# Performance work log

Measured on AMD Instinct MI355X. Metric: run time of the kernel, lower is better.

The kernel has to match this reference:

```python
import jax, jax.numpy as jnp
import numpy as np

HEADS = 16
DIM_HEAD = 64
SEG = 512            # total_segment_len (num_longterm_mem_tokens = 0)
THETA = 10000.0
NEG_INF = -1e30


def _rotate_half(t):
    # interleaved pair rotation, as in rotary-embedding-torch
    t2 = t.reshape(*t.shape[:-1], t.shape[-1] // 2, 2)
    return jnp.stack((-t2[..., 1], t2[..., 0]), axis=-1).reshape(t.shape)


def setup_inputs() -> dict:
    key = jax.random.key(0)
    ks = jax.random.split(key, 4)
    b, n, d = 2, 4096, 1024
    dim_inner = HEADS * DIM_HEAD
    seq = jax.random.normal(ks[0], (b, n, d), dtype=jnp.float32)
    g_norm = jnp.ones((d,), dtype=jnp.float32)
    W_qkv = jax.random.normal(ks[1], (d, 3 * dim_inner), dtype=jnp.float32) * (d ** -0.5)
    W_out = jax.random.normal(ks[2], (dim_inner, d), dtype=jnp.float32) * (dim_inner ** -0.5)
    pm = jax.random.normal(ks[3], (2, HEADS, 16, DIM_HEAD), dtype=jnp.float32) * 0.02
    return {"seq": seq, "g_norm": g_norm, "W_qkv": W_qkv, "W_out": W_out, "pm": pm}


def reference(seq, g_norm, W_qkv, W_out, pm):
    b, n_tot, dim = seq.shape
    p = pm.shape[2]
    dh = DIM_HEAD

    # RMSNorm (elementwise affine, eps = dtype eps as in torch default)
    eps = jnp.asarray(jnp.finfo(seq.dtype).eps, seq.dtype)
    x = seq * jax.lax.rsqrt(jnp.mean(seq * seq, axis=-1, keepdims=True) + eps) * g_norm

    qkv = x @ W_qkv                                   # [b, n, 3*h*dh]
    q, k, v = jnp.split(qkv, 3, axis=-1)

    def split_heads(t):
        return t.reshape(b, n_tot, HEADS, dh).transpose(0, 2, 1, 3)  # b h n d

    q, k, v = map(split_heads, (q, k, v))

    # rotary over global positions (applied before segmenting)
    pos = jnp.arange(n_tot, dtype=seq.dtype)
    inv_freq = 1.0 / (THETA ** (jnp.arange(0, dh, 2, dtype=seq.dtype) / dh))
    ang = jnp.repeat(pos[:, None] * inv_freq, 2, axis=-1)            # [n, dh]
    cos, sin = jnp.cos(ang), jnp.sin(ang)
    q = q * cos + _rotate_half(q) * sin
    k = k * cos + _rotate_half(k) * sin

    # fold segments into batch: b h (w n) d -> (b w) h n d
    w = n_tot // SEG
    def seg_fold(t):
        return t.reshape(b, HEADS, w, SEG, dh).transpose(0, 2, 1, 3, 4).reshape(b * w, HEADS, SEG, dh)
    q, k, v = map(seg_fold, (q, k, v))

    # prepend persistent memory kv
    pmk = jnp.broadcast_to(pm[0], (b * w, HEADS, p, dh))
    pmv = jnp.broadcast_to(pm[1], (b * w, HEADS, p, dh))
    k = jnp.concatenate((pmk, k), axis=-2)            # [(bw), h, p+n, d]
    v = jnp.concatenate((pmv, v), axis=-2)

    scores = jnp.einsum('bhid,bhjd->bhij', q, k) * (dh ** -0.5)
    i = jnp.arange(SEG)[:, None]
    j = jnp.arange(SEG + p)[None, :]
    mask = (j < p) | ((j - p) <= i)                   # persistent mem always visible, causal in-segment
    scores = jnp.where(mask, scores, NEG_INF)
    attn = jax.nn.softmax(scores, axis=-1)
    out = jnp.einsum('bhij,bhjd->bhid', attn, v)      # [(bw), h, n, d]

    out = out.transpose(0, 2, 1, 3).reshape(b * w, SEG, HEADS * dh)
    out = out @ W_out
    return out.reshape(b, n_tot, dim)
```

## Files before the change

### kernel.cpp

```cpp
#include <hip/hip_runtime.h>
#include <hip/hip_bf16.h>

typedef __attribute__((ext_vector_type(8))) short short8v;
typedef __attribute__((ext_vector_type(4))) float f32x4;

#define B_ 2
#define NTOK 4096
#define DMODEL 1024
#define HEADS_ 16
#define DH 64
#define SEG_ 512
#define PMEM 16
#define ROWS 8192
#define QKVC 3072

__global__ __launch_bounds__(256) void rmsnorm_bf16(const float* __restrict__ seq,
                                                    const float* __restrict__ g,
                                                    __hip_bfloat16* __restrict__ x) {
    int row = blockIdx.x;
    const float4* in = (const float4*)(seq + (size_t)row * DMODEL);
    int tid = threadIdx.x;
    float4 v = in[tid];
    float ss = v.x*v.x + v.y*v.y + v.z*v.z + v.w*v.w;
    #pragma unroll
    for (int off = 32; off >= 1; off >>= 1) ss += __shfl_xor(ss, off, 64);
    __shared__ float red[4];
    if ((tid & 63) == 0) red[tid >> 6] = ss;
    __syncthreads();
    float tot = red[0] + red[1] + red[2] + red[3];
    float scale = rsqrtf(tot * (1.0f/(float)DMODEL) + 1.1920929e-7f);
    float4 gv = ((const float4*)g)[tid];
    union { ushort4 u; __hip_bfloat16 h[4]; } pk;
    pk.h[0] = __float2bfloat16(v.x*scale*gv.x);
    pk.h[1] = __float2bfloat16(v.y*scale*gv.y);
    pk.h[2] = __float2bfloat16(v.z*scale*gv.z);
    pk.h[3] = __float2bfloat16(v.w*scale*gv.w);
    ((ushort4*)(x + (size_t)row * DMODEL))[tid] = pk.u;
}

__global__ __launch_bounds__(256) void setup_kernel(float* __restrict__ tab,
                                                    const float* __restrict__ pm,
                                                    __hip_bfloat16* __restrict__ pmb,
                                                    const float* __restrict__ wqkv,
                                                    __hip_bfloat16* __restrict__ wqkvt,
                                                    const float* __restrict__ wout,
                                                    __hip_bfloat16* __restrict__ woutt) {
    __shared__ float t[32][33];
    int b = blockIdx.x;
    if (b < 640) {
        int idx = b*256 + threadIdx.x;
        if (idx < NTOK*32) {
            int n = idx >> 5, p = idx & 31;
            float inv = powf(10000.f, -(float)p * (1.f/32.f));
            float a = (float)n * inv;
            float sn, cs;
            sincosf(a, &sn, &cs);
            tab[(size_t)n*64 + 2*p]     = cs;
            tab[(size_t)n*64 + 2*p + 1] = sn;
        } else {
            int j = idx - NTOK*32;
            pmb[j] = __float2bfloat16(pm[j]);
        }
        return;
    }
    b -= 640;
    const float* W; __hip_bfloat16* Wt; int N, n0, k0;
    if (b < 3072) { W = wqkv; Wt = wqkvt; N = QKVC;   n0 = (b % 96)*32; k0 = (b / 96)*32; }
    else { b -= 3072; W = wout; Wt = woutt; N = DMODEL; n0 = (b % 32)*32; k0 = (b / 32)*32; }
    int c = threadIdx.x & 31, r = threadIdx.x >> 5;
    #pragma unroll
    for (int rr = 0; rr < 32; rr += 8)
        t[rr + r][c] = W[(size_t)(k0 + rr + r)*N + n0 + c];
    __syncthreads();
    #pragma unroll
    for (int rr = 0; rr < 32; rr += 8)
        Wt[(size_t)(n0 + rr + r)*DMODEL + k0 + c] = __float2bfloat16(t[c][rr + r]);
}

__device__ __forceinline__ void gldl(const __hip_bfloat16* g, char* l) {
    __builtin_amdgcn_global_load_lds((const __attribute__((address_space(1))) void*)g,
                                     (__attribute__((address_space(3))) void*)l, 16, 0, 0);
}
__device__ __forceinline__ void storeC(float* p, float v) { *p = v; }
__device__ __forceinline__ void storeC(__hip_bfloat16* p, float v) { *p = __float2bfloat16(v); }

template<typename OutT, bool ROPE>
__global__ __launch_bounds__(256, 2) void gemm_t(const __hip_bfloat16* __restrict__ A,
                                                 const __hip_bfloat16* __restrict__ Bt,
                                                 OutT* __restrict__ C,
                                                 const float* __restrict__ tab,
                                                 int M, int N, int K) {
    __shared__ __align__(16) char smem[32768];
    const int tid = threadIdx.x;
    const int wid = tid >> 6, lane = tid & 63;
    const int q8 = gridDim.x >> 3;
    const int swz = (blockIdx.x & 7) * q8 + (blockIdx.x >> 3);
    const int nbx = N >> 7;
    const int bm = (swz / nbx) * 128, bn = (swz % nbx) * 128;
    const int wm = (wid >> 1) * 64, wn = (wid & 1) * 64;
    const int fr = lane & 15, g = lane >> 4;

    const int srow = tid >> 3;
    const int scol = ((tid & 7) ^ (srow & 7)) * 8;
    const __hip_bfloat16* Asrc = A  + (size_t)(bm + srow)*K + scol;
    const __hip_bfloat16* Bsrc = Bt + (size_t)(bn + srow)*K + scol;

    f32x4 acc[4][4];
    #pragma unroll
    for (int i = 0; i < 4; ++i)
        #pragma unroll
        for (int j = 0; j < 4; ++j)
            acc[i][j] = (f32x4){0.f, 0.f, 0.f, 0.f};

    for (int k0 = 0; k0 < K; k0 += 64) {
        #pragma unroll
        for (int i = 0; i < 4; ++i)
            gldl(Asrc + (size_t)i*32*K + k0, smem + i*4096 + tid*16);
        #pragma unroll
        for (int i = 0; i < 4; ++i)
            gldl(Bsrc + (size_t)i*32*K + k0, smem + 16384 + i*4096 + tid*16);
        __syncthreads();

        short8v a[4][2], b[4][2];
        #pragma unroll
        for (int mt = 0; mt < 4; ++mt) {
            int row = wm + mt*16 + fr;
            #pragma unroll
            for (int ks = 0; ks < 2; ++ks)
                a[mt][ks] = *(const short8v*)(smem + row*128 + ((ks*64 + g*16) ^ ((fr&7)<<4)));
        }
        #pragma unroll
        for (int nt = 0; nt < 4; ++nt) {
            int row = wn + nt*16 + fr;
            #pragma unroll
            for (int ks = 0; ks < 2; ++ks)
                b[nt][ks] = *(const short8v*)(smem + 16384 + row*128 + ((ks*64 + g*16) ^ ((fr&7)<<4)));
        }
        #pragma unroll
        for (int mt = 0; mt < 4; ++mt)
            #pragma unroll
            for (int nt = 0; nt < 4; ++nt)
                #pragma unroll
                for (int ks = 0; ks < 2; ++ks)
                    acc[mt][nt] = __builtin_amdgcn_mfma_f32_16x16x32_bf16(a[mt][ks], b[nt][ks], acc[mt][nt], 0, 0, 0);
        __syncthreads();
    }

    const int rsub = (lane >> 4) << 2;
    if (ROPE && bn < 2048) {
        #pragma unroll
        for (int mt = 0; mt < 4; ++mt) {
            int rbase = bm + wm + mt*16 + rsub;
            #pragma unroll
            for (int nt = 0; nt < 4; ++nt) {
                int col = bn + wn + nt*16 + fr;
                int d = col & 63;
                int dc = d & ~1;
                #pragma unroll
                for (int r = 0; r < 4; ++r) {
                    float v = acc[mt][nt][r];
                    float pv = __shfl_xor(v, 1, 64);
                    int n = (rbase + r) & (NTOK - 1);
                    const float* tb = tab + (size_t)n*64;
                    float cs = tb[dc], sn = tb[dc+1];
                    float o = v*cs + ((d & 1) ? pv*sn : -pv*sn);
                    storeC(&C[(size_t)(rbase + r)*N + col], (float)o);
                }
            }
        }
    } else {
        #pragma unroll
        for (int mt = 0; mt < 4; ++mt) {
            int rbase = bm + wm + mt*16 + rsub;
            #pragma unroll
            for (int nt = 0; nt < 4; ++nt) {
                int col = bn + wn + nt*16 + fr;
                #pragma unroll
                for (int r = 0; r < 4; ++r)
                    storeC(&C[(size_t)(rbase + r)*N + col], acc[mt][nt][r]);
            }
        }
    }
}

__device__ __forceinline__ void stage_load(const __hip_bfloat16* __restrict__ qkv,
                                           const __hip_bfloat16* __restrict__ pmb,
                                           int h, int srow, int tt, int skey, int sdg,
                                           uint4 kv[2]) {
    int kg = tt*64 + skey;
    if (kg < PMEM) {
        kv[0] = *(const uint4*)(pmb + ((size_t)h*PMEM + kg)*DH + sdg);
        kv[1] = *(const uint4*)(pmb + ((size_t)(HEADS_ + h)*PMEM + kg)*DH + sdg);
    } else {
        int r = min(kg - PMEM, SEG_ - 1);
        const __hip_bfloat16* bp = qkv + (size_t)(srow + r)*QKVC + h*DH + sdg;
        kv[0] = *(const uint4*)(bp + 1024);
        kv[1] = *(const uint4*)(bp + 2048);
    }
}

__device__ __forceinline__ void stage_write(char* Kb, char* Vb,
                                            int skey, int sdg, const uint4 kv[2]) {
    *(uint4*)(Kb + ((skey*128 + sdg*2) ^ ((skey&7)<<4))) = kv[0];
    union { uint4 u; ushort s[8]; } vv; vv.u = kv[1];
    #pragma unroll
    for (int j = 0; j < 8; ++j) {
        int d = sdg + j;
        *(ushort*)(Vb + ((d*128 + skey*2) ^ ((d&7)<<4))) = vv.s[j];
    }
}

__global__ __launch_bounds__(512, 2) void attn_mfma(const __hip_bfloat16* __restrict__ qkv,
                                                    const __hip_bfloat16* __restrict__ pmb,
                                                    __hip_bfloat16* __restrict__ ao) {
    __shared__ __hip_bfloat16 KB[2][4096];
    __shared__ __hip_bfloat16 VB[2][4096];
    __shared__ __hip_bfloat16 PB[8][1024];

    const int bid = blockIdx.x;
    const int xcd = bid & 7, ii = bid >> 3;
    const int s  = 2*xcd + (ii >> 5);
    const int h  = ii & 15;
    const int rb = (ii >> 4) & 1;
    const int srow = (s >> 3)*NTOK + (s & 7)*SEG_;
    const int tid = threadIdx.x;
    const int w = tid >> 6, lane = tid & 63;
    const int g = lane >> 4, fr = lane & 15;
    const int rsub = g * 4;
    char* Pw = (char*)&PB[w][0];

    const int grp0 = 2*w + rb;
    const int grp1 = 30 - 2*w + rb;
    const int tmax = 7 + rb;

    short8v aq[2][2];
    #pragma unroll
    for (int mt = 0; mt < 2; ++mt) {
        int grp = mt ? grp1 : grp0;
        const __hip_bfloat16* qp = qkv + (size_t)(srow + grp*16 + fr)*QKVC + h*DH;
        #pragma unroll
        for (int ks = 0; ks < 2; ++ks)
            aq[mt][ks] = *(const short8v*)(qp + ks*32 + g*8);
    }

    f32x4 accO[2][4];
    float l_[2][4];
    #pragma unroll
    for (int mt = 0; mt < 2; ++mt) {
        #pragma unroll
        for (int dt = 0; dt < 4; ++dt) accO[mt][dt] = (f32x4){0.f,0.f,0.f,0.f};
        #pragma unroll
        for (int r = 0; r < 4; ++r) l_[mt][r] = 0.f;
    }

    const int skey = tid >> 3, sdg = (tid & 7) * 8;

    {
        uint4 kv[2];
        stage_load(qkv, pmb, h, srow, 0, skey, sdg, kv);
        stage_write((char*)&KB[0][0], (char*)&VB[0][0], skey, sdg, kv);
    }
    __syncthreads();

    for (int t = 0; t <= tmax; ++t) {
        const int bf = t & 1;
        uint4 kvn[2];
        if (t < tmax) stage_load(qkv, pmb, h, srow, t + 1, skey, sdg, kvn);

        char* Kb = (char*)&KB[bf][0];
        char* Vb = (char*)&VB[bf][0];

        short8v bk[4][2];
        #pragma unroll
        for (int nt = 0; nt < 4; ++nt)
            #pragma unroll
            for (int ks = 0; ks < 2; ++ks) {
                int row = nt*16 + fr;
                bk[nt][ks] = *(const short8v*)(Kb + ((row*128 + ks*64 + g*16) ^ ((row&7)<<4)));
            }

        #pragma unroll
        for (int mt = 0; mt < 2; ++mt) {
            const int qb = (mt ? grp1 : grp0) * 16;
            if (t > 0 && t*64 > qb + 31) continue;

            f32x4 sA[4];
            #pragma unroll
            for (int nt = 0; nt < 4; ++nt) sA[nt] = (f32x4){0.f,0.f,0.f,0.f};
            __builtin_amdgcn_s_setprio(1);
            #pragma unroll
            for (int ks = 0; ks < 2; ++ks)
                #pragma unroll
                for (int nt = 0; nt < 4; ++nt)
                    sA[nt] = __builtin_amdgcn_mfma_f32_16x16x32_bf16(aq[mt][ks], bk[nt][ks], sA[nt], 0, 0, 0);
            __builtin_amdgcn_s_setprio(0);

            if (!(t*64 + 63 <= qb + 16)) {
                #pragma unroll
                for (int nt = 0; nt < 4; ++nt) {
                    int kg2 = t*64 + nt*16 + fr;
                    #pragma unroll
                    for (int r = 0; r < 4; ++r) {
                        int irow = qb + rsub + r;
                        if (!((kg2 < PMEM) || (kg2 <= irow + PMEM))) sA[nt][r] = -1e30f;
                    }
                }
            }

            #pragma unroll
            for (int nt = 0; nt < 4; ++nt)
                #pragma unroll
                for (int r = 0; r < 4; ++r)
                    sA[nt][r] = __expf(fmaf(sA[nt][r], 0.125f, -8.0f));
            #pragma unroll
            for (int r = 0; r < 4; ++r)
                l_[mt][r] += sA[0][r] + sA[1][r] + sA[2][r] + sA[3][r];

            #pragma unroll
            for (int nt = 0; nt < 4; ++nt)
                #pragma unroll
                for (int r = 0; r < 4; ++r) {
                    int row_l = rsub + r;
                    *(__hip_bfloat16*)(Pw + ((row_l*128 + (nt*16 + fr)*2) ^ ((row_l&7)<<4))) =
                        __float2bfloat16(sA[nt][r]);
                }

            __builtin_amdgcn_s_setprio(1);
            #pragma unroll
            for (int ks2 = 0; ks2 < 2; ++ks2) {
                short8v ap = *(const short8v*)(Pw + ((fr*128 + ks2*64 + g*16) ^ ((fr&7)<<4)));
                #pragma unroll
                for (int dt = 0; dt < 4; ++dt) {
                    int vrow = dt*16 + fr;
                    short8v bv = *(const short8v*)(Vb + ((vrow*128 + ks2*64 + g*16) ^ ((vrow&7)<<4)));
                    accO[mt][dt] = __builtin_amdgcn_mfma_f32_16x16x32_bf16(ap, bv, accO[mt][dt], 0, 0, 0);
                }
            }
            __builtin_amdgcn_s_setprio(0);
        }

        if (t < tmax) stage_write((char*)&KB[bf^1][0], (char*)&VB[bf^1][0], skey, sdg, kvn);
        __syncthreads();
    }

    #pragma unroll
    for (int mt = 0; mt < 2; ++mt) {
        const int grp = mt ? grp1 : grp0;
        float inv[4];
        #pragma unroll
        for (int r = 0; r < 4; ++r) {
            float lt = l_[mt][r];
            #pragma unroll
            for (int off = 1; off <= 8; off <<= 1) lt += __shfl_xor(lt, off, 64);
            inv[r] = 1.0f / lt;
        }
        #pragma unroll
        for (int dt = 0; dt < 4; ++dt)
            #pragma unroll
            for (int r = 0; r < 4; ++r) {
                int row_l = rsub + r;
                *(__hip_bfloat16*)(Pw + ((row_l*128 + (dt*16 + fr)*2) ^ ((row_l&7)<<4))) =
                    __float2bfloat16(accO[mt][dt][r] * inv[r]);
            }
        #pragma unroll
        for (int c = 0; c < 2; ++c) {
            int row_l = c*8 + (lane >> 3);
            size_t grow = (size_t)(srow + grp*16 + row_l);
            uint4 v = *(const uint4*)(Pw + ((row_l*128 + (lane&7)*16) ^ ((row_l&7)<<4)));
            *(uint4*)((char*)(ao + grow*DMODEL + h*DH) + (lane&7)*16) = v;
        }
    }
}

extern "C" void kernel_launch(void* const* d_in, const int* in_sizes, int n_in,
                              void* d_out, int out_size, void* d_ws, size_t ws_size,
                              hipStream_t stream) {
    const float* seq  = (const float*)d_in[0];
    const float* g    = (const float*)d_in[1];
    const float* wqkv = (const float*)d_in[2];
    const float* wout = (const float*)d_in[3];
    const float* pm   = (const float*)d_in[4];
    float* out = (float*)d_out;

    char* ws = (char*)d_ws;
    __hip_bfloat16* qkvb  = (__hip_bfloat16*)ws;
    __hip_bfloat16* xb    = (__hip_bfloat16*)(ws + 50331648);
    __hip_bfloat16* wqkvt = (__hip_bfloat16*)(ws + 50331648 + 16777216);
    __hip_bfloat16* woutt = (__hip_bfloat16*)(ws + 50331648 + 16777216 + 6291456);
    float* tab            = (float*)(ws + 50331648 + 16777216 + 6291456 + 2097152);
    __hip_bfloat16* pmb   = (__hip_bfloat16*)(ws + 50331648 + 16777216 + 6291456 + 2097152 + 1048576);

    setup_kernel<<<4736, 256, 0, stream>>>(tab, pm, pmb, wqkv, wqkvt, wout, woutt);
    rmsnorm_bf16<<<ROWS, 256, 0, stream>>>(seq, g, xb);
    gemm_t<__hip_bfloat16, true><<<(QKVC/128)*(ROWS/128), 256, 0, stream>>>(xb, wqkvt, qkvb, tab, ROWS, QKVC, DMODEL);
    attn_mfma<<<512, 512, 0, stream>>>(qkvb, pmb, xb);
    gemm_t<float, false><<<(DMODEL/128)*(ROWS/128), 256, 0, stream>>>(xb, woutt, out, nullptr, ROWS, DMODEL, DMODEL);
}
```

Before: 147.9 us.

## Merge setup and RMSNorm launches; stage 128-key K/V tiles in attention

Folds the one-time setup kernel and the RMSNorm kernel into a single launch, using block-index ranges to pick the role, which removes one launch and its inter-kernel gap. The attention kernel now stages 128 keys per pipeline step as two 64-key halves, so the number of loop iterations and __syncthreads barriers is halved. Each thread loads twice as much K/V per stage. Shared memory per block doubles to about 80 KB, which may limit occupancy at two blocks per CU.

```diff
diff --git a/kernel.cpp b/kernel.cpp
--- a/kernel.cpp
+++ b/kernel.cpp
@@ -14,49 +14,51 @@
 #define ROWS 8192
 #define QKVC 3072
 
-__global__ __launch_bounds__(256) void rmsnorm_bf16(const float* __restrict__ seq,
-                                                    const float* __restrict__ g,
-                                                    __hip_bfloat16* __restrict__ x) {
-    int row = blockIdx.x;
-    const float4* in = (const float4*)(seq + (size_t)row * DMODEL);
+__global__ __launch_bounds__(256) void prep_all(float* __restrict__ tab,
+                                                const float* __restrict__ pm,
+                                                __hip_bfloat16* __restrict__ pmb,
+                                                const float* __restrict__ wqkv,
+                                                __hip_bfloat16* __restrict__ wqkvt,
+                                                const float* __restrict__ wout,
+                                                __hip_bfloat16* __restrict__ woutt,
+                                                const float* __restrict__ seq,
+                                                const float* __restrict__ g,
+                                                __hip_bfloat16* __restrict__ x) {
+    __shared__ float t[32][33];
+    __shared__ float red[4];
+    int b = blockIdx.x;
     int tid = threadIdx.x;
-    float4 v = in[tid];
-    float ss = v.x*v.x + v.y*v.y + v.z*v.z + v.w*v.w;
-    #pragma unroll
-    for (int off = 32; off >= 1; off >>= 1) ss += __shfl_xor(ss, off, 64);
-    __shared__ float red[4];
-    if ((tid & 63) == 0) red[tid >> 6] = ss;
-    __syncthreads();
-    float tot = red[0] + red[1] + red[2] + red[3];
-    float scale = rsqrtf(tot * (1.0f/(float)DMODEL) + 1.1920929e-7f);
-    float4 gv = ((const float4*)g)[tid];
-    union { ushort4 u; __hip_bfloat16 h[4]; } pk;
-    pk.h[0] = __float2bfloat16(v.x*scale*gv.x);
-    pk.h[1] = __float2bfloat16(v.y*scale*gv.y);
-    pk.h[2] = __float2bfloat16(v.z*scale*gv.z);
-    pk.h[3] = __float2bfloat16(v.w*scale*gv.w);
-    ((ushort4*)(x + (size_t)row * DMODEL))[tid] = pk.u;
-}
-
-__global__ __launch_bounds__(256) void setup_kernel(float* __restrict__ tab,
-                                                    const float* __restrict__ pm,
-                                                    __hip_bfloat16* __restrict__ pmb,
-                                                    const float* __restrict__ wqkv,
-                                                    __hip_bfloat16* __restrict__ wqkvt,
-                                                    const float* __restrict__ wout,
-                                                    __hip_bfloat16* __restrict__ woutt) {
-    __shared__ float t[32][33];
-    int b = blockIdx.x;
+    if (b >= 4736) {
+        int row = b - 4736;
+        const float4* in = (const float4*)(seq + (size_t)row * DMODEL);
+        float4 v = in[tid];
+        float ss = v.x*v.x + v.y*v.y + v.z*v.z + v.w*v.w;
+        #pragma unroll
+        for (int off = 32; off >= 1; off >>= 1) ss += __shfl_xor(ss, off, 64);
+        if ((tid & 63) == 0) red[tid >> 6] = ss;
+        __syncthreads();
+        float tot = red[0] + red[1] + red[2] + red[3];
+        float scale = rsqrtf(tot * (1.0f/(float)DMODEL) + 1.1920929e-7f);
+        float4 gv = ((const float4*)g)[tid];
+        union { ushort4 u; __hip_bfloat16 h[4]; } pk;
+        pk.h[0] = __float2bfloat16(v.x*scale*gv.x);
+        pk.h[1] = __float2bfloat16(v.y*scale*gv.y);
+        pk.h[2] = __float2bfloat16(v.z*scale*gv.z);
+        pk.h[3] = __float2bfloat16(v.w*scale*gv.w);
+        ((ushort4*)(x + (size_t)row * DMODEL))[tid] = pk.u;
+        return;
+    }
     if (b < 640) {
-        int idx = b*256 + threadIdx.x;
+        int idx = b*256 + tid;
         if (idx < NTOK*32) {
             int n = idx >> 5, p = idx & 31;
             float inv = powf(10000.f, -(float)p * (1.f/32.f));
             float a = (float)n * inv;
             float sn, cs;
             sincosf(a, &sn, &cs);
-            tab[(size_t)n*64 + 2*p]     = cs;
-            tab[(size_t)n*64 + 2*p + 1] = sn;
+            float* tp = tab + (size_t)n*64;
+            tp[2*p]     = cs;
+            tp[2*p + 1] = sn;
         } else {
             int j = idx - NTOK*32;
             pmb[j] = __float2bfloat16(pm[j]);
@@ -67,7 +69,7 @@
     const float* W; __hip_bfloat16* Wt; int N, n0, k0;
     if (b < 3072) { W = wqkv; Wt = wqkvt; N = QKVC;   n0 = (b % 96)*32; k0 = (b / 96)*32; }
     else { b -= 3072; W = wout; Wt = woutt; N = DMODEL; n0 = (b % 32)*32; k0 = (b / 32)*32; }
-    int c = threadIdx.x & 31, r = threadIdx.x >> 5;
+    int c = tid & 31, r = tid >> 5;
     #pragma unroll
     for (int rr = 0; rr < 32; rr += 8)
         t[rr + r][c] = W[(size_t)(k0 + rr + r)*N + n0 + c];
@@ -186,35 +188,42 @@
 __device__ __forceinline__ void stage_load(const __hip_bfloat16* __restrict__ qkv,
                                            const __hip_bfloat16* __restrict__ pmb,
                                            int h, int srow, int tt, int skey, int sdg,
-                                           uint4 kv[2]) {
-    int kg = tt*64 + skey;
+                                           uint4 kv[4]) {
+    int kg = tt*128 + skey;
     if (kg < PMEM) {
-        kv[0] = *(const uint4*)(pmb + ((size_t)h*PMEM + kg)*DH + sdg);
-        kv[1] = *(const uint4*)(pmb + ((size_t)(HEADS_ + h)*PMEM + kg)*DH + sdg);
+        const __hip_bfloat16* kp = pmb + ((size_t)h*PMEM + kg)*DH + sdg;
+        const __hip_bfloat16* vp = pmb + ((size_t)(HEADS_ + h)*PMEM + kg)*DH + sdg;
+        kv[0] = *(const uint4*)kp;      kv[1] = *(const uint4*)(kp + 8);
+        kv[2] = *(const uint4*)vp;      kv[3] = *(const uint4*)(vp + 8);
     } else {
         int r = min(kg - PMEM, SEG_ - 1);
         const __hip_bfloat16* bp = qkv + (size_t)(srow + r)*QKVC + h*DH + sdg;
-        kv[0] = *(const uint4*)(bp + 1024);
-        kv[1] = *(const uint4*)(bp + 2048);
+        kv[0] = *(const uint4*)(bp + 1024); kv[1] = *(const uint4*)(bp + 1032);
+        kv[2] = *(const uint4*)(bp + 2048); kv[3] = *(const uint4*)(bp + 2056);
     }
 }
 
 __device__ __forceinline__ void stage_write(char* Kb, char* Vb,
-                                            int skey, int sdg, const uint4 kv[2]) {
-    *(uint4*)(Kb + ((skey*128 + sdg*2) ^ ((skey&7)<<4))) = kv[0];
-    union { uint4 u; ushort s[8]; } vv; vv.u = kv[1];
-    #pragma unroll
-    for (int j = 0; j < 8; ++j) {
+                                            int skey, int sdg, const uint4 kv[4]) {
+    int half = skey >> 6, row = skey & 63;
+    char* Kh = Kb + half*8192;
+    int b0 = row*128 + sdg*2;
+    *(uint4*)(Kh + ((b0)      ^ ((row&7)<<4))) = kv[0];
+    *(uint4*)(Kh + ((b0 + 16) ^ ((row&7)<<4))) = kv[1];
+    char* Vh = Vb + half*8192;
+    union { uint4 u[2]; ushort s[16]; } vv; vv.u[0] = kv[2]; vv.u[1] = kv[3];
+    #pragma unroll
+    for (int j = 0; j < 16; ++j) {
         int d = sdg + j;
-        *(ushort*)(Vb + ((d*128 + skey*2) ^ ((d&7)<<4))) = vv.s[j];
+        *(ushort*)(Vh + ((d*128 + row*2) ^ ((d&7)<<4))) = vv.s[j];
     }
 }
 
 __global__ __launch_bounds__(512, 2) void attn_mfma(const __hip_bfloat16* __restrict__ qkv,
                                                     const __hip_bfloat16* __restrict__ pmb,
                                                     __hip_bfloat16* __restrict__ ao) {
-    __shared__ __hip_bfloat16 KB[2][4096];
-    __shared__ __hip_bfloat16 VB[2][4096];
+    __shared__ __hip_bfloat16 KB[2][8192];
+    __shared__ __hip_bfloat16 VB[2][8192];
     __shared__ __hip_bfloat16 PB[8][1024];
 
     const int bid = blockIdx.x;
@@ -231,7 +240,7 @@
 
     const int grp0 = 2*w + rb;
     const int grp1 = 30 - 2*w + rb;
-    const int tmax = 7 + rb;
+    const int tmax = 3 + rb;
 
     short8v aq[2][2];
     #pragma unroll
@@ -253,10 +262,10 @@
         for (int r = 0; r < 4; ++r) l_[mt][r] = 0.f;
     }
 
-    const int skey = tid >> 3, sdg = (tid & 7) * 8;
+    const int skey = tid >> 2, sdg = (tid & 3) * 16;
 
     {
-        uint4 kv[2];
+        uint4 kv[4];
         stage_load(qkv, pmb, h, srow, 0, skey, sdg, kv);
         stage_write((char*)&KB[0][0], (char*)&VB[0][0], skey, sdg, kv);
     }
@@ -264,79 +273,83 @@
 
     for (int t = 0; t <= tmax; ++t) {
         const int bf = t & 1;
-        uint4 kvn[2];
+        uint4 kvn[4];
         if (t < tmax) stage_load(qkv, pmb, h, srow, t + 1, skey, sdg, kvn);
 
-        char* Kb = (char*)&KB[bf][0];
-        char* Vb = (char*)&VB[bf][0];
-
-        short8v bk[4][2];
-        #pragma unroll
-        for (int nt = 0; nt < 4; ++nt)
-            #pragma unroll
-            for (int ks = 0; ks < 2; ++ks) {
-                int row = nt*16 + fr;
-                bk[nt][ks] = *(const short8v*)(Kb + ((row*128 + ks*64 + g*16) ^ ((row&7)<<4)));
-            }
-
-        #pragma unroll
-        for (int mt = 0; mt < 2; ++mt) {
-            const int qb = (mt ? grp1 : grp0) * 16;
-            if (t > 0 && t*64 > qb + 31) continue;
-
-            f32x4 sA[4];
-            #pragma unroll
-            for (int nt = 0; nt < 4; ++nt) sA[nt] = (f32x4){0.f,0.f,0.f,0.f};
-            __builtin_amdgcn_s_setprio(1);
-            #pragma unroll
-            for (int ks = 0; ks < 2; ++ks)
+        #pragma unroll
+        for (int hs = 0; hs < 2; ++hs) {
+            char* Kb = (char*)&KB[bf][0] + hs*8192;
+            char* Vb = (char*)&VB[bf][0] + hs*8192;
+            const int base = t*128 + hs*64;
+
+            short8v bk[4][2];
+            #pragma unroll
+            for (int nt = 0; nt < 4; ++nt)
+                #pragma unroll
+                for (int ks = 0; ks < 2; ++ks) {
+                    int row = nt*16 + fr;
+                    bk[nt][ks] = *(const short8v*)(Kb + ((row*128 + ks*64 + g*16) ^ ((row&7)<<4)));
+                }
+
+            #pragma unroll
+            for (int mt = 0; mt < 2; ++mt) {
+                const int qb = (mt ? grp1 : grp0) * 16;
+                if (base > 0 && base > qb + 31) continue;
+
+                f32x4 sA[4];
+                #pragma unroll
+                for (int nt = 0; nt < 4; ++nt) sA[nt] = (f32x4){0.f,0.f,0.f,0.f};
+                __builtin_amdgcn_s_setprio(1);
+                #pragma unroll
+                for (int ks = 0; ks < 2; ++ks)
+                    #pragma unroll
+                    for (int nt = 0; nt < 4; ++nt)
+                        sA[nt] = __builtin_amdgcn_mfma_f32_16x16x32_bf16(aq[mt][ks], bk[nt][ks], sA[nt], 0, 0, 0);
+                __builtin_amdgcn_s_setprio(0);
+
+                if (!(base + 63 <= qb + 16)) {
+                    #pragma unroll
+                    for (int nt = 0; nt < 4; ++nt) {
+                        int kg2 = base + nt*16 + fr;
+                        #pragma unroll
+                        for (int r = 0; r < 4; ++r) {
+                            int irow = qb + rsub + r;
+                            if (!((kg2 < PMEM) || (kg2 <= irow + PMEM))) sA[nt][r] = -1e30f;
+                        }
+                    }
+                }
+
                 #pragma unroll
                 for (int nt = 0; nt < 4; ++nt)
-                    sA[nt] = __builtin_amdgcn_mfma_f32_16x16x32_bf16(aq[mt][ks], bk[nt][ks], sA[nt], 0, 0, 0);
-            __builtin_amdgcn_s_setprio(0);
-
-            if (!(t*64 + 63 <= qb + 16)) {
-                #pragma unroll
-                for (int nt = 0; nt < 4; ++nt) {
-                    int kg2 = t*64 + nt*16 + fr;
+                    #pragma unroll
+                    for (int r = 0; r < 4; ++r)
+                        sA[nt][r] = __expf(fmaf(sA[nt][r], 0.125f, -8.0f));
+                #pragma unroll
+                for (int r = 0; r < 4; ++r)
+                    l_[mt][r] += sA[0][r] + sA[1][r] + sA[2][r] + sA[3][r];
+
+                #pragma unroll
+                for (int nt = 0; nt < 4; ++nt)
                     #pragma unroll
                     for (int r = 0; r < 4; ++r) {
-                        int irow = qb + rsub + r;
-                        if (!((kg2 < PMEM) || (kg2 <= irow + PMEM))) sA[nt][r] = -1e30f;
+                        int row_l = rsub + r;
+                        *(__hip_bfloat16*)(Pw + ((row_l*128 + (nt*16 + fr)*2) ^ ((row_l&7)<<4))) =
+                            __float2bfloat16(sA[nt][r]);
+                    }
+
+                __builtin_amdgcn_s_setprio(1);
+                #pragma unroll
+                for (int ks2 = 0; ks2 < 2; ++ks2) {
+                    short8v ap = *(const short8v*)(Pw + ((fr*128 + ks2*64 + g*16) ^ ((fr&7)<<4)));
+                    #pragma unroll
+                    for (int dt = 0; dt < 4; ++dt) {
+                        int vrow = dt*16 + fr;
+                        short8v bv = *(const short8v*)(Vb + ((vrow*128 + ks2*64 + g*16) ^ ((vrow&7)<<4)));
+                        accO[mt][dt] = __builtin_amdgcn_mfma_f32_16x16x32_bf16(ap, bv, accO[mt][dt], 0, 0, 0);
                     }
                 }
+                __builtin_amdgcn_s_setprio(0);
             }
-
-            #pragma unroll
-            for (int nt = 0; nt < 4; ++nt)
-                #pragma unroll
-                for (int r = 0; r < 4; ++r)
-                    sA[nt][r] = __expf(fmaf(sA[nt][r], 0.125f, -8.0f));
-            #pragma unroll
-            for (int r = 0; r < 4; ++r)
-                l_[mt][r] += sA[0][r] + sA[1][r] + sA[2][r] + sA[3][r];
-
-            #pragma unroll
-            for (int nt = 0; nt < 4; ++nt)
-                #pragma unroll
-                for (int r = 0; r < 4; ++r) {
-                    int row_l = rsub + r;
-                    *(__hip_bfloat16*)(Pw + ((row_l*128 + (nt*16 + fr)*2) ^ ((row_l&7)<<4))) =
-                        __float2bfloat16(sA[nt][r]);
-                }
-
-            __builtin_amdgcn_s_setprio(1);
-            #pragma unroll
-            for (int ks2 = 0; ks2 < 2; ++ks2) {
-                short8v ap = *(const short8v*)(Pw + ((fr*128 + ks2*64 + g*16) ^ ((fr&7)<<4)));
-                #pragma unroll
-                for (int dt = 0; dt < 4; ++dt) {
-                    int vrow = dt*16 + fr;
-                    short8v bv = *(const short8v*)(Vb + ((vrow*128 + ks2*64 + g*16) ^ ((vrow&7)<<4)));
-                    accO[mt][dt] = __builtin_amdgcn_mfma_f32_16x16x32_bf16(ap, bv, accO[mt][dt], 0, 0, 0);
-                }
-            }
-            __builtin_amdgcn_s_setprio(0);
         }
 
         if (t < tmax) stage_write((char*)&KB[bf^1][0], (char*)&VB[bf^1][0], skey, sdg, kvn);
@@ -390,8 +403,7 @@
     float* tab            = (float*)(ws + 50331648 + 16777216 + 6291456 + 2097152);
     __hip_bfloat16* pmb   = (__hip_bfloat16*)(ws + 50331648 + 16777216 + 6291456 + 2097152 + 1048576);
 
-    setup_kernel<<<4736, 256, 0, stream>>>(tab, pm, pmb, wqkv, wqkvt, wout, woutt);
-    rmsnorm_bf16<<<ROWS, 256, 0, stream>>>(seq, g, xb);
+    prep_all<<<12928, 256, 0, stream>>>(tab, pm, pmb, wqkv, wqkvt, wout, woutt, seq, g, xb);
     gemm_t<__hip_bfloat16, true><<<(QKVC/128)*(ROWS/128), 256, 0, stream>>>(xb, wqkvt, qkvb, tab, ROWS, QKVC, DMODEL);
     attn_mfma<<<512, 512, 0, stream>>>(qkvb, pmb, xb);
     gemm_t<float, false><<<(DMODEL/128)*(ROWS/128), 256, 0, stream>>>(xb, woutt, out, nullptr, ROWS, DMODEL, DMODEL);
```

New measurement: 149.1 us. About the same (+0.8%).
